# Kernel tuning notes

Hardware: AMD Instinct MI355X
Metric: run time of the kernel (lower is better)

## Reference

```python
import jax, jax.numpy as jnp
import numpy as np
from jax import lax

B, CIN, COUT, H, W = 4, 256, 256, 64, 64
KH = KW = 3
K = KH * KW
GN_GROUPS = 32
EPS = 1e-5


def setup_inputs() -> dict:
    key = jax.random.key(0)
    ks = jax.random.split(key, 6)
    x = jax.random.normal(ks[0], (B, CIN, H, W), jnp.float32)
    # offset predictor conv: 3x3, 18 out channels, with bias (init small so offsets stay near 0)
    offset_w = jax.random.normal(ks[1], (2 * K, CIN, KH, KW), jnp.float32) * 0.01
    offset_b = jax.random.normal(ks[2], (2 * K,), jnp.float32) * 0.01
    # deformable conv weight (no bias), He-ish scale
    deform_w = jax.random.normal(ks[3], (COUT, CIN, KH, KW), jnp.float32) * (1.0 / np.sqrt(CIN * K))
    gn_gamma = jnp.ones((COUT,), jnp.float32)
    gn_beta = jnp.zeros((COUT,), jnp.float32)
    return {"x": x, "offset_w": offset_w, "offset_b": offset_b,
            "deform_w": deform_w, "gn_gamma": gn_gamma, "gn_beta": gn_beta}


def _deform_conv(x, offset, weight):
    """Deformable conv v1, stride=1, pad=1, dil=1, deformable_groups=1.
    x: [B,C,H,W]; offset: [B,2K,H,W] with (dy,dx) per kernel tap; weight: [O,C,3,3].
    """
    b, c, h, w = x.shape
    off = offset.reshape(b, K, 2, h, w)
    # base sampling grid per kernel tap: p = p0 - pad + k
    ky, kx = jnp.meshgrid(jnp.arange(KH), jnp.arange(KW), indexing="ij")
    base_y = (jnp.arange(h, dtype=jnp.float32) - 1.0)[None, :, None] + ky.reshape(K).astype(jnp.float32)[:, None, None]  # [K,H,1]
    base_x = (jnp.arange(w, dtype=jnp.float32) - 1.0)[None, None, :] + kx.reshape(K).astype(jnp.float32)[:, None, None]  # [K,1,W]
    py = base_y[None] + off[:, :, 0]  # [B,K,H,W]
    px = base_x[None] + off[:, :, 1]  # [B,K,H,W]

    y0 = jnp.floor(py)
    x0 = jnp.floor(px)
    ty = py - y0
    tx = px - x0
    y0 = y0.astype(jnp.int32)
    x0 = x0.astype(jnp.int32)

    x_hw = x.transpose(0, 2, 3, 1).reshape(b, h * w, c)  # [B,HW,C]

    def corner(yi, xi, wgt):
        valid = (yi >= 0) & (yi < h) & (xi >= 0) & (xi < w)
        yc = jnp.clip(yi, 0, h - 1)
        xc = jnp.clip(xi, 0, w - 1)
        idx = (yc * w + xc).reshape(b, K * h * w)
        v = jnp.take_along_axis(x_hw, idx[..., None], axis=1)  # [B,KHW,C]
        return v * (wgt * valid.astype(wgt.dtype)).reshape(b, K * h * w, 1)

    samp = (corner(y0, x0, (1 - ty) * (1 - tx))
            + corner(y0, x0 + 1, (1 - ty) * tx)
            + corner(y0 + 1, x0, ty * (1 - tx))
            + corner(y0 + 1, x0 + 1, ty * tx))  # [B,KHW,C]
    samp = samp.reshape(b, K, h, w, c)
    return jnp.einsum("bkhwc,ock->bohw", samp, weight.reshape(weight.shape[0], c, K))


def reference(x, offset_w, offset_b, deform_w, gn_gamma, gn_beta):
    # offset = conv3x3(x) + bias
    offset = lax.conv_general_dilated(
        x, offset_w, window_strides=(1, 1), padding=((1, 1), (1, 1)),
        dimension_numbers=("NCHW", "OIHW", "NCHW")) + offset_b[None, :, None, None]
    out = _deform_conv(x, offset, deform_w)
    # GroupNorm(32, COUT) + ReLU
    b, c, h, w = out.shape
    g = out.reshape(b, GN_GROUPS, (c // GN_GROUPS) * h * w)
    mu = g.mean(axis=2, keepdims=True)
    var = g.var(axis=2, keepdims=True)
    g = (g - mu) * lax.rsqrt(var + EPS)
    out = g.reshape(b, c, h, w) * gn_gamma[None, :, None, None] + gn_beta[None, :, None, None]
    return jax.nn.relu(out)
```

## Files before the change

kernel.cpp:

```cpp
#include <hip/hip_runtime.h>
#include <hip/hip_bf16.h>
#include <stdint.h>


typedef unsigned short u16;
typedef __bf16 bf16x8 __attribute__((ext_vector_type(8)));
typedef float f32x4_t __attribute__((ext_vector_type(4)));

#define HW 4096

__device__ __forceinline__ uint32_t f32_to_bf16_rne(float f) {
  uint32_t u = __builtin_bit_cast(uint32_t, f);
  return (u + 0x7FFFu + ((u >> 16) & 1u)) >> 16;
}
__device__ __forceinline__ float bf_lo(uint32_t u) {
  return __builtin_bit_cast(float, u << 16);
}
__device__ __forceinline__ float bf_hi(uint32_t u) {
  return __builtin_bit_cast(float, u & 0xFFFF0000u);
}

__global__ __launch_bounds__(256) void k_transpose(const float* __restrict__ x,
                                                   u16* __restrict__ xt) {
  __shared__ float tile[32][33];
  int b = blockIdx.z;
  int c0 = blockIdx.y * 32;
  int p0 = blockIdx.x * 32;
  int tx = threadIdx.x, ty = threadIdx.y;
#pragma unroll
  for (int j = 0; j < 32; j += 8)
    tile[ty + j][tx] = x[(b * 256 + c0 + ty + j) * HW + p0 + tx];
  __syncthreads();
  int wid = ty * 32 + tx;
  int cp = wid & 15;
  int pr = wid >> 4;
#pragma unroll
  for (int j = 0; j < 2; j++) {
    int p = pr + j * 16;
    uint32_t lo = f32_to_bf16_rne(tile[cp * 2][p]);
    uint32_t hi = f32_to_bf16_rne(tile[cp * 2 + 1][p]);
    *(uint32_t*)&xt[(b * HW + p0 + p) * 256 + c0 + cp * 2] = lo | (hi << 16);
  }
}

__global__ __launch_bounds__(256) void k_prep_w(const float* __restrict__ wsrc,
                                                u16* __restrict__ warr) {
  int e = blockIdx.x * 256 + threadIdx.x;
  int kk = e & 7, m = (e >> 3) & 255, g = (e >> 11) & 7, kc = e >> 14;
  int cin = (kc & 3) * 64 + g * 8 + kk;
  int tap = kc >> 2;
  float v = wsrc[m * 2304 + cin * 9 + tap];
  warr[e] = (u16)f32_to_bf16_rne(v);
}

__global__ __launch_bounds__(256) void k_prep_owm(const float* __restrict__ ow,
                                                  u16* __restrict__ owm) {
  int e = blockIdx.x * 256 + threadIdx.x;
  int kk = e & 7, m = (e >> 3) & 31, g = (e >> 8) & 7, kc = e >> 11;
  int cin = (kc & 3) * 64 + g * 8 + kk;
  int tap = kc >> 2;
  float v = (m < 18) ? ow[m * 2304 + cin * 9 + tap] : 0.f;
  owm[e] = (u16)f32_to_bf16_rne(v);
}

__global__ __launch_bounds__(256) void k_conv(
    const u16* __restrict__ xt, const u16* __restrict__ warr,
    const u16* __restrict__ owm, const float* __restrict__ ob,
    float* __restrict__ out) {
  __shared__ char smem[27136];
  u16* stage = (u16*)smem;
  float* off_part = (float*)(smem + 16896);
  int4* ci_s = (int4*)smem;
  float4* mw_s = (float4*)(smem + 4608);
  u16* b_s = (u16*)(smem + 16896);

  int tid = threadIdx.x;
  int lane = tid & 63;
  int wm = tid >> 6;
  int b = blockIdx.x >> 7;
  int pt = blockIdx.x & 127;
  int p0 = pt * 32;
  int yrow = p0 >> 6, xbase = p0 & 63;

  {
    u16* st = stage + wm * 2112;
    int q = lane & 15, pq = lane >> 4;
    f32x4_t a2[2][2] = {};
#pragma unroll 1
    for (int tap = wm; tap < 9; tap += 4) {
      int ky = tap / 3, kx = tap % 3;
      int yy = yrow + ky - 1;
      bool vy = (yy >= 0) && (yy < 64);
#pragma unroll
      for (int cc = 0; cc < 4; cc++) {
        int kc = tap * 4 + cc;
#pragma unroll
        for (int i = 0; i < 8; i++) {
          int px = i * 4 + pq;
          int xx2 = xbase + px + kx - 1;
          uint2 v = make_uint2(0u, 0u);
          if (vy && xx2 >= 0 && xx2 < 64)
            v = *(const uint2*)&xt[(b * HW + yy * 64 + xx2) * 256 + cc * 64 + q * 4];
          *(uint2*)&st[(q >> 1) * 264 + px * 8 + (q & 1) * 4] = v;
        }
#pragma unroll
        for (int ks = 0; ks < 2; ks++) {
          int g = ks * 4 + pq;
          const u16* ab = owm + kc * 2048 + g * 256;
#pragma unroll
          for (int s = 0; s < 2; s++) {
            bf16x8 bfr = *(bf16x8*)&st[g * 264 + (s * 16 + q) * 8];
#pragma unroll
            for (int im = 0; im < 2; im++) {
              bf16x8 af = *(const bf16x8*)&ab[(im * 16 + q) * 8];
              a2[s][im] = __builtin_amdgcn_mfma_f32_16x16x32_bf16(af, bfr, a2[s][im], 0, 0, 0);
            }
          }
        }
      }
    }
#pragma unroll
    for (int s = 0; s < 2; s++)
#pragma unroll
      for (int im = 0; im < 2; im++)
#pragma unroll
        for (int r = 0; r < 4; r++) {
          int oc = im * 16 + pq * 4 + r;
          if (oc < 18) off_part[(wm * 32 + s * 16 + q) * 20 + oc] = a2[s][im][r];
        }
  }
  __syncthreads();
  for (int it = tid; it < 288; it += 256) {
    int tap = it >> 5;
    int px = it & 31;
    float dy = ob[2 * tap], dx = ob[2 * tap + 1];
#pragma unroll
    for (int wv = 0; wv < 4; wv++) {
      dy += off_part[(wv * 32 + px) * 20 + 2 * tap];
      dx += off_part[(wv * 32 + px) * 20 + 2 * tap + 1];
    }
    int ky = tap / 3, kx = tap % 3;
    int p = p0 + px;
    int yq = p >> 6, xq = p & 63;
    float py = (float)(yq - 1 + ky) + dy;
    float pxx = (float)(xq - 1 + kx) + dx;
    float y0f = floorf(py), x0f = floorf(pxx);
    float ty = py - y0f, tx = pxx - x0f;
    int y0 = (int)y0f, x0 = (int)x0f;
    int y1 = y0 + 1, x1 = x0 + 1;
    float wy0 = 1.f - ty, wy1 = ty, wx0 = 1.f - tx, wx1 = tx;
    bool vy0 = (y0 >= 0) && (y0 < 64), vy1 = (y1 >= 0) && (y1 < 64);
    bool vx0 = (x0 >= 0) && (x0 < 64), vx1 = (x1 >= 0) && (x1 < 64);
    int cy0 = min(max(y0, 0), 63), cy1 = min(max(y1, 0), 63);
    int cx0 = min(max(x0, 0), 63), cx1 = min(max(x1, 0), 63);
    int base = b * HW;
    int4 ci;
    ci.x = (base + cy0 * 64 + cx0) * 256;
    ci.y = (base + cy0 * 64 + cx1) * 256;
    ci.z = (base + cy1 * 64 + cx0) * 256;
    ci.w = (base + cy1 * 64 + cx1) * 256;
    float4 mw;
    mw.x = wy0 * wx0 * ((vy0 && vx0) ? 1.f : 0.f);
    mw.y = wy0 * wx1 * ((vy0 && vx1) ? 1.f : 0.f);
    mw.z = wy1 * wx0 * ((vy1 && vx0) ? 1.f : 0.f);
    mw.w = wy1 * wx1 * ((vy1 && vx1) ? 1.f : 0.f);
    ci_s[it] = ci;
    mw_s[it] = mw;
  }
  __syncthreads();

  int q = tid & 15, pxb = (tid >> 4) & 15;
  f32x4_t acc[2][4] = {};
#pragma unroll 1
  for (int tap = 0; tap < 9; tap++) {
    int4 ci0 = ci_s[tap * 32 + pxb];
    int4 ci1 = ci_s[tap * 32 + 16 + pxb];
    float4 mw0 = mw_s[tap * 32 + pxb];
    float4 mw1 = mw_s[tap * 32 + 16 + pxb];
#pragma unroll
    for (int cc = 0; cc < 4; cc++) {
      int kc = tap * 4 + cc;
      int e = cc * 64 + q * 4;
      u16* bb = b_s + (kc & 1) * 2176;
      {
        uint2 c0v = *(const uint2*)&xt[ci0.x + e];
        uint2 c1v = *(const uint2*)&xt[ci0.y + e];
        uint2 c2v = *(const uint2*)&xt[ci0.z + e];
        uint2 c3v = *(const uint2*)&xt[ci0.w + e];
        float r0 = mw0.x * bf_lo(c0v.x) + mw0.y * bf_lo(c1v.x) + mw0.z * bf_lo(c2v.x) + mw0.w * bf_lo(c3v.x);
        float r1 = mw0.x * bf_hi(c0v.x) + mw0.y * bf_hi(c1v.x) + mw0.z * bf_hi(c2v.x) + mw0.w * bf_hi(c3v.x);
        float r2 = mw0.x * bf_lo(c0v.y) + mw0.y * bf_lo(c1v.y) + mw0.z * bf_lo(c2v.y) + mw0.w * bf_lo(c3v.y);
        float r3 = mw0.x * bf_hi(c0v.y) + mw0.y * bf_hi(c1v.y) + mw0.z * bf_hi(c2v.y) + mw0.w * bf_hi(c3v.y);
        uint2 u;
        u.x = f32_to_bf16_rne(r0) | (f32_to_bf16_rne(r1) << 16);
        u.y = f32_to_bf16_rne(r2) | (f32_to_bf16_rne(r3) << 16);
        *(uint2*)&bb[(q >> 1) * 136 + pxb * 8 + (q & 1) * 4] = u;
      }
      {
        uint2 c0v = *(const uint2*)&xt[ci1.x + e];
        uint2 c1v = *(const uint2*)&xt[ci1.y + e];
        uint2 c2v = *(const uint2*)&xt[ci1.z + e];
        uint2 c3v = *(const uint2*)&xt[ci1.w + e];
        float r0 = mw1.x * bf_lo(c0v.x) + mw1.y * bf_lo(c1v.x) + mw1.z * bf_lo(c2v.x) + mw1.w * bf_lo(c3v.x);
        float r1 = mw1.x * bf_hi(c0v.x) + mw1.y * bf_hi(c1v.x) + mw1.z * bf_hi(c2v.x) + mw1.w * bf_hi(c3v.x);
        float r2 = mw1.x * bf_lo(c0v.y) + mw1.y * bf_lo(c1v.y) + mw1.z * bf_lo(c2v.y) + mw1.w * bf_lo(c3v.y);
        float r3 = mw1.x * bf_hi(c0v.y) + mw1.y * bf_hi(c1v.y) + mw1.z * bf_hi(c2v.y) + mw1.w * bf_hi(c3v.y);
        uint2 u;
        u.x = f32_to_bf16_rne(r0) | (f32_to_bf16_rne(r1) << 16);
        u.y = f32_to_bf16_rne(r2) | (f32_to_bf16_rne(r3) << 16);
        *(uint2*)&bb[1088 + (q >> 1) * 136 + pxb * 8 + (q & 1) * 4] = u;
      }
      __syncthreads();
#pragma unroll
      for (int ks = 0; ks < 2; ks++) {
        int g = ks * 4 + (lane >> 4);
        bf16x8 b0 = *(bf16x8*)&bb[g * 136 + (lane & 15) * 8];
        bf16x8 b1 = *(bf16x8*)&bb[1088 + g * 136 + (lane & 15) * 8];
        const u16* ab = warr + kc * 16384 + g * 2048 + (wm * 64 + (lane & 15)) * 8;
#pragma unroll
        for (int im = 0; im < 4; im++) {
          bf16x8 af = *(const bf16x8*)&ab[im * 128];
          acc[0][im] = __builtin_amdgcn_mfma_f32_16x16x32_bf16(af, b0, acc[0][im], 0, 0, 0);
          acc[1][im] = __builtin_amdgcn_mfma_f32_16x16x32_bf16(af, b1, acc[1][im], 0, 0, 0);
        }
      }
    }
  }
  int rq = lane >> 4;
#pragma unroll
  for (int s = 0; s < 2; s++) {
    int n = p0 + s * 16 + (lane & 15);
#pragma unroll
    for (int im = 0; im < 4; im++)
#pragma unroll
      for (int r = 0; r < 4; r++) {
        int m = wm * 64 + im * 16 + rq * 4 + r;
        out[(b * 256 + m) * HW + n] = acc[s][im][r];
      }
  }
}

__global__ __launch_bounds__(256) void k_gn_part(const float* __restrict__ out,
                                                 float2* __restrict__ part) {
  int blk = blockIdx.x;
  int bg = blk >> 2, qt = blk & 3;
  const float4* base = (const float4*)(out + (size_t)bg * 32768 + (size_t)qt * 8192);
  int tid = threadIdx.x;
  float s = 0.f, ss = 0.f;
#pragma unroll
  for (int i = 0; i < 8; i++) {
    float4 v = base[tid + i * 256];
    s += v.x + v.y + v.z + v.w;
    ss += v.x * v.x + v.y * v.y + v.z * v.z + v.w * v.w;
  }
#pragma unroll
  for (int m = 1; m < 64; m <<= 1) {
    s += __shfl_xor(s, m);
    ss += __shfl_xor(ss, m);
  }
  __shared__ float ls[4], lss[4];
  int wv = tid >> 6, lane = tid & 63;
  if (lane == 0) { ls[wv] = s; lss[wv] = ss; }
  __syncthreads();
  if (tid == 0)
    part[blk] = make_float2(ls[0] + ls[1] + ls[2] + ls[3],
                            lss[0] + lss[1] + lss[2] + lss[3]);
}

__global__ __launch_bounds__(256) void k_gn_apply(float* __restrict__ out,
                                                  const float2* __restrict__ part,
                                                  const float* __restrict__ gamma,
                                                  const float* __restrict__ beta) {
  __shared__ float sga, sbe;
  int gid = blockIdx.x * 256 + threadIdx.x;
  int c = (gid >> 10) & 255;
  int bb = gid >> 18;
  if (threadIdx.x == 0) {
    int p4 = (bb * 32 + (c >> 3)) * 4;
    float s = 0.f, ss = 0.f;
#pragma unroll
    for (int j = 0; j < 4; j++) {
      float2 p = part[p4 + j];
      s += p.x;
      ss += p.y;
    }
    float mu = s / 32768.f;
    float var = ss / 32768.f - mu * mu;
    float rs = rsqrtf(var + 1e-5f);
    float ga = gamma[c] * rs;
    sga = ga;
    sbe = beta[c] - mu * ga;
  }
  __syncthreads();
  float ga = sga, be = sbe;
  float4 v = ((const float4*)out)[gid];
  v.x = fmaxf(v.x * ga + be, 0.f);
  v.y = fmaxf(v.y * ga + be, 0.f);
  v.z = fmaxf(v.z * ga + be, 0.f);
  v.w = fmaxf(v.w * ga + be, 0.f);
  ((float4*)out)[gid] = v;
}

extern "C" void kernel_launch(void* const* d_in, const int* in_sizes, int n_in,
                              void* d_out, int out_size, void* d_ws, size_t ws_size,
                              hipStream_t stream) {
  const float* x = (const float*)d_in[0];
  const float* offset_w = (const float*)d_in[1];
  const float* offset_b = (const float*)d_in[2];
  const float* deform_w = (const float*)d_in[3];
  const float* gn_gamma = (const float*)d_in[4];
  const float* gn_beta = (const float*)d_in[5];
  float* out = (float*)d_out;
  char* ws = (char*)d_ws;

  u16* xt = (u16*)ws;
  u16* warr = (u16*)(ws + 8388608);
  u16* owm = (u16*)(ws + 9568256);
  float2* part = (float2*)(ws + 9715712);

  k_transpose<<<dim3(128, 8, 4), dim3(32, 8), 0, stream>>>(x, xt);
  k_prep_w<<<dim3(2304), dim3(256), 0, stream>>>(deform_w, warr);
  k_prep_owm<<<dim3(288), dim3(256), 0, stream>>>(offset_w, owm);
  k_conv<<<dim3(512), dim3(256), 0, stream>>>(xt, warr, owm, offset_b, out);
  k_gn_part<<<dim3(512), dim3(256), 0, stream>>>(out, part);
  k_gn_apply<<<dim3(4096), dim3(256), 0, stream>>>(out, part, gn_gamma, gn_beta);
}
```

Baseline: 172.1 us.

## Double conv block to 512 threads, fuse GroupNorm stats via atomics, merge prep kernels

Raises the conv kernel to 512 threads (8 waves), so each thread gathers one bilinear sample per tap instead of two and each wave owns 32 output channels. GroupNorm partial sums now come straight from the conv accumulators through wave shuffles and atomicAdd into a zeroed buffer, which removes the separate stats kernel and its re-read of the output. The two weight-prep kernels are merged into one launch that also zeroes the stats buffer. Costs are more shared memory per block, float atomics whose summation order varies between runs, and one-pass variance in fp32.

```diff
diff --git a/kernel.cpp b/kernel.cpp
--- a/kernel.cpp
+++ b/kernel.cpp
@@ -43,36 +43,41 @@
   }
 }
 
-__global__ __launch_bounds__(256) void k_prep_w(const float* __restrict__ wsrc,
-                                                u16* __restrict__ warr) {
-  int e = blockIdx.x * 256 + threadIdx.x;
-  int kk = e & 7, m = (e >> 3) & 255, g = (e >> 11) & 7, kc = e >> 14;
-  int cin = (kc & 3) * 64 + g * 8 + kk;
-  int tap = kc >> 2;
-  float v = wsrc[m * 2304 + cin * 9 + tap];
-  warr[e] = (u16)f32_to_bf16_rne(v);
-}
-
-__global__ __launch_bounds__(256) void k_prep_owm(const float* __restrict__ ow,
-                                                  u16* __restrict__ owm) {
-  int e = blockIdx.x * 256 + threadIdx.x;
-  int kk = e & 7, m = (e >> 3) & 31, g = (e >> 8) & 7, kc = e >> 11;
-  int cin = (kc & 3) * 64 + g * 8 + kk;
-  int tap = kc >> 2;
-  float v = (m < 18) ? ow[m * 2304 + cin * 9 + tap] : 0.f;
-  owm[e] = (u16)f32_to_bf16_rne(v);
-}
-
-__global__ __launch_bounds__(256) void k_conv(
+__global__ __launch_bounds__(256) void k_prep(const float* __restrict__ wsrc,
+                                              const float* __restrict__ ow,
+                                              u16* __restrict__ warr,
+                                              u16* __restrict__ owm,
+                                              float* __restrict__ part) {
+  int bid = blockIdx.x;
+  int tid = threadIdx.x;
+  if (bid < 2304) {
+    int e = bid * 256 + tid;
+    int kk = e & 7, m = (e >> 3) & 255, g = (e >> 11) & 7, kc = e >> 14;
+    int cin = (kc & 3) * 64 + g * 8 + kk;
+    int tap = kc >> 2;
+    warr[e] = (u16)f32_to_bf16_rne(wsrc[m * 2304 + cin * 9 + tap]);
+  } else if (bid < 2592) {
+    int e = (bid - 2304) * 256 + tid;
+    int kk = e & 7, m = (e >> 3) & 31, g = (e >> 8) & 7, kc = e >> 11;
+    int cin = (kc & 3) * 64 + g * 8 + kk;
+    int tap = kc >> 2;
+    float v = (m < 18) ? ow[m * 2304 + cin * 9 + tap] : 0.f;
+    owm[e] = (u16)f32_to_bf16_rne(v);
+  } else {
+    part[tid] = 0.f;
+  }
+}
+
+__global__ __launch_bounds__(512, 4) void k_conv(
     const u16* __restrict__ xt, const u16* __restrict__ warr,
     const u16* __restrict__ owm, const float* __restrict__ ob,
-    float* __restrict__ out) {
-  __shared__ char smem[27136];
+    float* __restrict__ out, float* __restrict__ part) {
+  __shared__ char smem[54272];
   u16* stage = (u16*)smem;
-  float* off_part = (float*)(smem + 16896);
+  float* off_part = (float*)(smem + 33792);
   int4* ci_s = (int4*)smem;
   float4* mw_s = (float4*)(smem + 4608);
-  u16* b_s = (u16*)(smem + 16896);
+  u16* b_s = (u16*)(smem + 9216);
 
   int tid = threadIdx.x;
   int lane = tid & 63;
@@ -87,7 +92,7 @@
     int q = lane & 15, pq = lane >> 4;
     f32x4_t a2[2][2] = {};
 #pragma unroll 1
-    for (int tap = wm; tap < 9; tap += 4) {
+    for (int tap = wm; tap < 9; tap += 8) {
       int ky = tap / 3, kx = tap % 3;
       int yy = yrow + ky - 1;
       bool vy = (yy >= 0) && (yy < 64);
@@ -130,12 +135,12 @@
         }
   }
   __syncthreads();
-  for (int it = tid; it < 288; it += 256) {
-    int tap = it >> 5;
-    int px = it & 31;
+  if (tid < 288) {
+    int tap = tid >> 5;
+    int px = tid & 31;
     float dy = ob[2 * tap], dx = ob[2 * tap + 1];
 #pragma unroll
-    for (int wv = 0; wv < 4; wv++) {
+    for (int wv = 0; wv < 8; wv++) {
       dy += off_part[(wv * 32 + px) * 20 + 2 * tap];
       dx += off_part[(wv * 32 + px) * 20 + 2 * tap + 1];
     }
@@ -164,51 +169,37 @@
     mw.y = wy0 * wx1 * ((vy0 && vx1) ? 1.f : 0.f);
     mw.z = wy1 * wx0 * ((vy1 && vx0) ? 1.f : 0.f);
     mw.w = wy1 * wx1 * ((vy1 && vx1) ? 1.f : 0.f);
-    ci_s[it] = ci;
-    mw_s[it] = mw;
+    ci_s[tid] = ci;
+    mw_s[tid] = mw;
   }
   __syncthreads();
 
-  int q = tid & 15, pxb = (tid >> 4) & 15;
-  f32x4_t acc[2][4] = {};
+  int q = tid & 15;
+  int pxb = tid >> 4;
+  int sub = pxb >> 4, pxs = pxb & 15;
+  f32x4_t acc[2][2] = {};
 #pragma unroll 1
   for (int tap = 0; tap < 9; tap++) {
-    int4 ci0 = ci_s[tap * 32 + pxb];
-    int4 ci1 = ci_s[tap * 32 + 16 + pxb];
-    float4 mw0 = mw_s[tap * 32 + pxb];
-    float4 mw1 = mw_s[tap * 32 + 16 + pxb];
+    int4 ci = ci_s[tap * 32 + pxb];
+    float4 mw4 = mw_s[tap * 32 + pxb];
 #pragma unroll
     for (int cc = 0; cc < 4; cc++) {
       int kc = tap * 4 + cc;
       int e = cc * 64 + q * 4;
       u16* bb = b_s + (kc & 1) * 2176;
       {
-        uint2 c0v = *(const uint2*)&xt[ci0.x + e];
-        uint2 c1v = *(const uint2*)&xt[ci0.y + e];
-        uint2 c2v = *(const uint2*)&xt[ci0.z + e];
-        uint2 c3v = *(const uint2*)&xt[ci0.w + e];
-        float r0 = mw0.x * bf_lo(c0v.x) + mw0.y * bf_lo(c1v.x) + mw0.z * bf_lo(c2v.x) + mw0.w * bf_lo(c3v.x);
-        float r1 = mw0.x * bf_hi(c0v.x) + mw0.y * bf_hi(c1v.x) + mw0.z * bf_hi(c2v.x) + mw0.w * bf_hi(c3v.x);
-        float r2 = mw0.x * bf_lo(c0v.y) + mw0.y * bf_lo(c1v.y) + mw0.z * bf_lo(c2v.y) + mw0.w * bf_lo(c3v.y);
-        float r3 = mw0.x * bf_hi(c0v.y) + mw0.y * bf_hi(c1v.y) + mw0.z * bf_hi(c2v.y) + mw0.w * bf_hi(c3v.y);
+        uint2 c0v = *(const uint2*)&xt[ci.x + e];
+        uint2 c1v = *(const uint2*)&xt[ci.y + e];
+        uint2 c2v = *(const uint2*)&xt[ci.z + e];
+        uint2 c3v = *(const uint2*)&xt[ci.w + e];
+        float r0 = mw4.x * bf_lo(c0v.x) + mw4.y * bf_lo(c1v.x) + mw4.z * bf_lo(c2v.x) + mw4.w * bf_lo(c3v.x);
+        float r1 = mw4.x * bf_hi(c0v.x) + mw4.y * bf_hi(c1v.x) + mw4.z * bf_hi(c2v.x) + mw4.w * bf_hi(c3v.x);
+        float r2 = mw4.x * bf_lo(c0v.y) + mw4.y * bf_lo(c1v.y) + mw4.z * bf_lo(c2v.y) + mw4.w * bf_lo(c3v.y);
+        float r3 = mw4.x * bf_hi(c0v.y) + mw4.y * bf_hi(c1v.y) + mw4.z * bf_hi(c2v.y) + mw4.w * bf_hi(c3v.y);
         uint2 u;
         u.x = f32_to_bf16_rne(r0) | (f32_to_bf16_rne(r1) << 16);
         u.y = f32_to_bf16_rne(r2) | (f32_to_bf16_rne(r3) << 16);
-        *(uint2*)&bb[(q >> 1) * 136 + pxb * 8 + (q & 1) * 4] = u;
-      }
-      {
-        uint2 c0v = *(const uint2*)&xt[ci1.x + e];
-        uint2 c1v = *(const uint2*)&xt[ci1.y + e];
-        uint2 c2v = *(const uint2*)&xt[ci1.z + e];
-        uint2 c3v = *(const uint2*)&xt[ci1.w + e];
-        float r0 = mw1.x * bf_lo(c0v.x) + mw1.y * bf_lo(c1v.x) + mw1.z * bf_lo(c2v.x) + mw1.w * bf_lo(c3v.x);
-        float r1 = mw1.x * bf_hi(c0v.x) + mw1.y * bf_hi(c1v.x) + mw1.z * bf_hi(c2v.x) + mw1.w * bf_hi(c3v.x);
-        float r2 = mw1.x * bf_lo(c0v.y) + mw1.y * bf_lo(c1v.y) + mw1.z * bf_lo(c2v.y) + mw1.w * bf_lo(c3v.y);
-        float r3 = mw1.x * bf_hi(c0v.y) + mw1.y * bf_hi(c1v.y) + mw1.z * bf_hi(c2v.y) + mw1.w * bf_hi(c3v.y);
-        uint2 u;
-        u.x = f32_to_bf16_rne(r0) | (f32_to_bf16_rne(r1) << 16);
-        u.y = f32_to_bf16_rne(r2) | (f32_to_bf16_rne(r3) << 16);
-        *(uint2*)&bb[1088 + (q >> 1) * 136 + pxb * 8 + (q & 1) * 4] = u;
+        *(uint2*)&bb[sub * 1088 + (q >> 1) * 136 + pxs * 8 + (q & 1) * 4] = u;
       }
       __syncthreads();
 #pragma unroll
@@ -216,9 +207,9 @@
         int g = ks * 4 + (lane >> 4);
         bf16x8 b0 = *(bf16x8*)&bb[g * 136 + (lane & 15) * 8];
         bf16x8 b1 = *(bf16x8*)&bb[1088 + g * 136 + (lane & 15) * 8];
-        const u16* ab = warr + kc * 16384 + g * 2048 + (wm * 64 + (lane & 15)) * 8;
-#pragma unroll
-        for (int im = 0; im < 4; im++) {
+        const u16* ab = warr + kc * 16384 + g * 2048 + (wm * 32 + (lane & 15)) * 8;
+#pragma unroll
+        for (int im = 0; im < 2; im++) {
           bf16x8 af = *(const bf16x8*)&ab[im * 128];
           acc[0][im] = __builtin_amdgcn_mfma_f32_16x16x32_bf16(af, b0, acc[0][im], 0, 0, 0);
           acc[1][im] = __builtin_amdgcn_mfma_f32_16x16x32_bf16(af, b1, acc[1][im], 0, 0, 0);
@@ -231,44 +222,39 @@
   for (int s = 0; s < 2; s++) {
     int n = p0 + s * 16 + (lane & 15);
 #pragma unroll
-    for (int im = 0; im < 4; im++)
+    for (int im = 0; im < 2; im++)
 #pragma unroll
       for (int r = 0; r < 4; r++) {
-        int m = wm * 64 + im * 16 + rq * 4 + r;
+        int m = wm * 32 + im * 16 + rq * 4 + r;
         out[(b * 256 + m) * HW + n] = acc[s][im][r];
       }
   }
-}
-
-__global__ __launch_bounds__(256) void k_gn_part(const float* __restrict__ out,
-                                                 float2* __restrict__ part) {
-  int blk = blockIdx.x;
-  int bg = blk >> 2, qt = blk & 3;
-  const float4* base = (const float4*)(out + (size_t)bg * 32768 + (size_t)qt * 8192);
-  int tid = threadIdx.x;
-  float s = 0.f, ss = 0.f;
-#pragma unroll
-  for (int i = 0; i < 8; i++) {
-    float4 v = base[tid + i * 256];
-    s += v.x + v.y + v.z + v.w;
-    ss += v.x * v.x + v.y * v.y + v.z * v.z + v.w * v.w;
-  }
-#pragma unroll
-  for (int m = 1; m < 64; m <<= 1) {
-    s += __shfl_xor(s, m);
-    ss += __shfl_xor(ss, m);
-  }
-  __shared__ float ls[4], lss[4];
-  int wv = tid >> 6, lane = tid & 63;
-  if (lane == 0) { ls[wv] = s; lss[wv] = ss; }
-  __syncthreads();
-  if (tid == 0)
-    part[blk] = make_float2(ls[0] + ls[1] + ls[2] + ls[3],
-                            lss[0] + lss[1] + lss[2] + lss[3]);
+#pragma unroll
+  for (int im = 0; im < 2; im++) {
+    float s = 0.f, ss = 0.f;
+#pragma unroll
+    for (int sb = 0; sb < 2; sb++)
+#pragma unroll
+      for (int r = 0; r < 4; r++) {
+        float v = acc[sb][im][r];
+        s += v;
+        ss += v * v;
+      }
+#pragma unroll
+    for (int mk = 1; mk < 32; mk <<= 1) {
+      s += __shfl_xor(s, mk);
+      ss += __shfl_xor(ss, mk);
+    }
+    if ((lane & 31) == 0) {
+      int grp = wm * 4 + im * 2 + (lane >> 5);
+      atomicAdd(&part[b * 32 + grp], s);
+      atomicAdd(&part[128 + b * 32 + grp], ss);
+    }
+  }
 }
 
 __global__ __launch_bounds__(256) void k_gn_apply(float* __restrict__ out,
-                                                  const float2* __restrict__ part,
+                                                  const float* __restrict__ part,
                                                   const float* __restrict__ gamma,
                                                   const float* __restrict__ beta) {
   __shared__ float sga, sbe;
@@ -276,14 +262,9 @@
   int c = (gid >> 10) & 255;
   int bb = gid >> 18;
   if (threadIdx.x == 0) {
-    int p4 = (bb * 32 + (c >> 3)) * 4;
-    float s = 0.f, ss = 0.f;
-#pragma unroll
-    for (int j = 0; j < 4; j++) {
-      float2 p = part[p4 + j];
-      s += p.x;
-      ss += p.y;
-    }
+    int bg = bb * 32 + (c >> 3);
+    float s = part[bg];
+    float ss = part[128 + bg];
     float mu = s / 32768.f;
     float var = ss / 32768.f - mu * mu;
     float rs = rsqrtf(var + 1e-5f);
@@ -316,12 +297,10 @@
   u16* xt = (u16*)ws;
   u16* warr = (u16*)(ws + 8388608);
   u16* owm = (u16*)(ws + 9568256);
-  float2* part = (float2*)(ws + 9715712);
+  float* part = (float*)(ws + 9715712);
 
   k_transpose<<<dim3(128, 8, 4), dim3(32, 8), 0, stream>>>(x, xt);
-  k_prep_w<<<dim3(2304), dim3(256), 0, stream>>>(deform_w, warr);
-  k_prep_owm<<<dim3(288), dim3(256), 0, stream>>>(offset_w, owm);
-  k_conv<<<dim3(512), dim3(256), 0, stream>>>(xt, warr, owm, offset_b, out);
-  k_gn_part<<<dim3(512), dim3(256), 0, stream>>>(out, part);
+  k_prep<<<dim3(2593), dim3(256), 0, stream>>>(deform_w, offset_w, warr, owm, part);
+  k_conv<<<dim3(512), dim3(512), 0, stream>>>(xt, warr, owm, offset_b, out, part);
   k_gn_apply<<<dim3(4096), dim3(256), 0, stream>>>(out, part, gn_gamma, gn_beta);
 }
```

Result: slower. 185.2 us (+7.6%).
